# Performance work log

Measured on AMD Instinct MI355X. Metric: run time of the kernel, lower is better.

Reference implementation:

```python
import jax, jax.numpy as jnp
from jax import lax
import numpy as np

B, H, W = 2, 48, 48
C_IN, C_OUT = 96, 192
D_INNER, N_STATE, DT_RANK, K = 192, 16, 6, 4  # VMamba: expand=2, d_state=16, dt_rank=ceil(C/16)
EPS = 1e-5


def setup_inputs() -> dict:
    ks = jax.random.split(jax.random.key(0), 16)
    s = 0.02
    r = lambda k, sh, sc=s: jax.random.normal(k, sh, jnp.float32) * sc
    d, N, R = D_INNER, N_STATE, DT_RANK
    return {
        "x": jax.random.normal(ks[0], (B, C_IN, H, W), jnp.float32),
        "ln_g": jnp.ones((C_IN,), jnp.float32),
        "ln_b": jnp.zeros((C_IN,), jnp.float32),
        "in_proj_w": r(ks[1], (2 * d, C_IN)),
        "dwconv_w": r(ks[2], (d, 1, 3, 3)),
        "dwconv_b": jnp.zeros((d,), jnp.float32),
        "x_proj_w": r(ks[3], (K, R + 2 * N, d)),
        "dt_w": r(ks[4], (K, d, R)),
        "dt_b": r(ks[5], (K, d), 0.1),
        "A_logs": jnp.tile(jnp.log(jnp.arange(1, N + 1, dtype=jnp.float32)), (K, d, 1)),
        "Ds": jnp.ones((K, d), jnp.float32),
        "out_norm_g": jnp.ones((d,), jnp.float32),
        "out_norm_b": jnp.zeros((d,), jnp.float32),
        "out_proj_w": r(ks[6], (C_IN, d)),
        "w1": r(ks[7], (C_OUT, C_IN, 1, 1)),
        "b1": jnp.zeros((C_OUT,), jnp.float32),
        "w31": r(ks[8], (C_OUT, C_IN, 3, 3)),
        "b31": jnp.zeros((C_OUT,), jnp.float32),
        "w32": r(ks[9], (C_OUT, C_IN, 3, 3)),
        "b32": jnp.zeros((C_OUT,), jnp.float32),
        "w33": r(ks[10], (C_OUT, C_OUT, 3, 3)),
        "b33": jnp.zeros((C_OUT,), jnp.float32),
        "bn_g": jnp.ones((3 * C_OUT,), jnp.float32),
        "bn_b": jnp.zeros((3 * C_OUT,), jnp.float32),
        "bn_m": r(ks[11], (3 * C_OUT,), 0.1),
        "bn_v": jax.random.uniform(ks[12], (3 * C_OUT,), jnp.float32) + 0.5,
        "prelu_a": jnp.float32(0.25),
    }


def _layernorm(x, g, b):
    m = jnp.mean(x, -1, keepdims=True)
    v = jnp.var(x, -1, keepdims=True)
    return (x - m) * lax.rsqrt(v + EPS) * g + b


def _conv(x, w, b, stride, pad, groups=1):
    y = lax.conv_general_dilated(x, w, (stride, stride), [(pad, pad), (pad, pad)],
                                 dimension_numbers=("NCHW", "OIHW", "NCHW"),
                                 feature_group_count=groups)
    return y + b[None, :, None, None]


def _ss2d(x, in_proj_w, dwconv_w, dwconv_b, x_proj_w, dt_w, dt_b, A_logs, Ds,
          out_norm_g, out_norm_b, out_proj_w):
    # x: (B, H, W, C)
    Bb, Hh, Ww, C = x.shape
    d, N, R = D_INNER, N_STATE, DT_RANK
    L = Hh * Ww
    xz = jnp.einsum("bhwc,ec->bhwe", x, in_proj_w)  # (B,H,W,2d)
    xin, z = jnp.split(xz, 2, axis=-1)
    xc = jnp.transpose(xin, (0, 3, 1, 2))           # (B,d,H,W)
    xc = jax.nn.silu(_conv(xc, dwconv_w, dwconv_b, 1, 1, groups=d))
    # 4 scan directions: row-major, col-major, and their reverses
    x_flat = xc.reshape(Bb, d, L)
    x_t = jnp.transpose(xc, (0, 1, 3, 2)).reshape(Bb, d, L)
    xs = jnp.stack([x_flat, x_t, x_flat[:, :, ::-1], x_t[:, :, ::-1]], axis=1)  # (B,K,d,L)
    x_dbl = jnp.einsum("bkdl,kcd->bkcl", xs, x_proj_w)
    dts, Bs, Cs = x_dbl[:, :, :R], x_dbl[:, :, R:R + N], x_dbl[:, :, R + N:]
    delta = jax.nn.softplus(jnp.einsum("bkrl,kdr->bkdl", dts, dt_w) + dt_b[None, :, :, None])
    A = -jnp.exp(A_logs)                                   # (K,d,N)
    dA = jnp.exp(jnp.einsum("bkdl,kdn->lbkdn", delta, A))  # (L,B,K,d,N)
    dBu = jnp.einsum("bkdl,bknl,bkdl->lbkdn", delta, Bs, xs)
    Cseq = jnp.transpose(Cs, (3, 0, 1, 2))                 # (L,B,K,N)

    def step(h, inp):
        dA_t, dBu_t, c_t = inp
        h = dA_t * h + dBu_t
        return h, jnp.einsum("bkdn,bkn->bkd", h, c_t)

    h0 = jnp.zeros((Bb, K, d, N), x.dtype)
    _, ys = lax.scan(step, h0, (dA, dBu, Cseq))            # ys: (L,B,K,d)
    ys = jnp.transpose(ys, (1, 2, 3, 0)) + xs * Ds[None, :, :, None]  # (B,K,d,L)

    def t_back(a):  # undo the HW transpose of col-major scans
        return jnp.transpose(a.reshape(Bb, d, Ww, Hh), (0, 1, 3, 2)).reshape(Bb, d, L)

    y = ys[:, 0] + ys[:, 2, :, ::-1] + t_back(ys[:, 1]) + t_back(ys[:, 3, :, ::-1])
    y = _layernorm(jnp.transpose(y, (0, 2, 1)), out_norm_g, out_norm_b).reshape(Bb, Hh, Ww, d)
    y = y * jax.nn.silu(z)
    return jnp.einsum("bhwd,cd->bhwc", y, out_proj_w)


def reference(x, ln_g, ln_b, in_proj_w, dwconv_w, dwconv_b, x_proj_w, dt_w, dt_b,
              A_logs, Ds, out_norm_g, out_norm_b, out_proj_w,
              w1, b1, w31, b31, w32, b32, w33, b33,
              bn_g, bn_b, bn_m, bn_v, prelu_a):
    # VSSBlock: residual + SS2D on LayerNorm'd NHWC features
    x_nhwc = jnp.transpose(x, (0, 2, 3, 1))
    x_nhwc = x_nhwc + _ss2d(_layernorm(x_nhwc, ln_g, ln_b), in_proj_w, dwconv_w,
                            dwconv_b, x_proj_w, dt_w, dt_b, A_logs, Ds,
                            out_norm_g, out_norm_b, out_proj_w)
    xm = jnp.transpose(x_nhwc, (0, 3, 1, 2))  # (B,C,H,W)
    # multi-branch stride-2 downsample
    x1 = _conv(xm, w1, b1, 2, 0)
    x2 = _conv(xm, w31, b31, 2, 1)
    x3 = _conv(_conv(xm, w32, b32, 2, 1), w33, b33, 1, 1)
    out = jnp.concatenate([x1, x2, x3], axis=1)  # (B, 3*C_OUT, H/2, W/2)
    # BatchNorm2d (inference, running stats) + PReLU(single param)
    out = (out - bn_m[None, :, None, None]) * lax.rsqrt(bn_v + EPS)[None, :, None, None] \
          * bn_g[None, :, None, None] + bn_b[None, :, None, None]
    return jnp.where(out > 0, out, prelu_a * out)
```

## Files before the change

### kernel.cpp

```cpp
#include <hip/hip_runtime.h>
#include <math.h>

#define BB_ 2
#define HH 48
#define WW 48
#define LL 2304
#define CIN 96
#define DD 192
#define KK 4
#define NN 16
#define RR 6
#define NCH 96
#define LC 24
#define COUT 192
#define OH 24
#define OW 24
#define OHW 576
#define NPX 1152
#define NTOT 4608
#define EPSF 1e-5f

typedef __attribute__((ext_vector_type(8))) short bf16x8;
typedef __attribute__((ext_vector_type(4))) float f32x4;

__device__ __forceinline__ short f2bf(float f) {
  unsigned u = __float_as_uint(f);
  unsigned r = (u + 0x7fffu + ((u >> 16) & 1u)) >> 16;
  return (short)r;
}

__global__ __launch_bounds__(256) void k_prep(const float* __restrict__ x,
                                              const float* __restrict__ g,
                                              const float* __restrict__ b,
                                              const float* __restrict__ inw,
                                              const float* __restrict__ xpw,
                                              const float* __restrict__ w31,
                                              const float* __restrict__ w32,
                                              const float* __restrict__ w33,
                                              const float* __restrict__ w1,
                                              const float* __restrict__ wout,
                                              float* __restrict__ stats,
                                              short* __restrict__ WgTb,
                                              float* __restrict__ sWg,
                                              float* __restrict__ sWb,
                                              short* __restrict__ At3p,
                                              short* __restrict__ At1b,
                                              short* __restrict__ At2b,
                                              short* __restrict__ woutb,
                                              short* __restrict__ xb) {
  __shared__ float tile[32][33];
  int bx = blockIdx.x;
  int tid = threadIdx.x;
  if (bx < 72) {
    int bb = bx / 36; int l0 = (bx % 36) * 64;
    int p = tid >> 2, q = tid & 3;
    int l = l0 + p;
    const float* xp = x + bb * CIN * LL + l;
    float s = 0.f, ss = 0.f;
    for (int c = q; c < CIN; c += 4) { float v = xp[c * LL]; s += v; ss += v * v; }
    s += __shfl_xor(s, 1, 64); s += __shfl_xor(s, 2, 64);
    ss += __shfl_xor(ss, 1, 64); ss += __shfl_xor(ss, 2, 64);
    if (q == 0) {
      float m = s / CIN; float var = ss / CIN - m * m;
      stats[(bb * LL + l) * 2 + 0] = m;
      stats[(bb * LL + l) * 2 + 1] = rsqrtf(var + EPSF);
    }
  } else if (bx == 72) {
    for (int e = tid; e < 2 * DD; e += 256) {
      float swg = 0.f, swb = 0.f;
      for (int c = 0; c < CIN; c++) {
        float w = inw[e * CIN + c];
        float wg = w * g[c];
        WgTb[e * CIN + c] = f2bf(wg);
        swg += wg; swb += w * b[c];
      }
      sWg[e] = swg; sWb[e] = swb;
    }
  } else if (bx < 217) {
    int idx = (bx - 73) * 256 + tid;
    if (idx < 4 * 48 * 192) {
      int m = idx / 192, d = idx - m * 192;
      int kd = m / 48, r = m - kd * 48;
      At3p[idx] = (r < 38) ? f2bf(xpw[(kd * 38 + r) * 192 + d]) : (short)0;
    }
  } else if (bx < 2161) {
    int i = (bx - 217) * 256 + tid;
    if (i < 497664) {
      float v;
      if (i < 165888) v = w31[i];
      else if (i < 331776) v = w32[i - 165888];
      else {
        int k = i % 864; int m = i / 864 - 384;
        v = (k % 9 == 4) ? w1[m * 96 + k / 9] : 0.f;
      }
      At1b[i] = f2bf(v);
    }
  } else if (bx < 3457) {
    int i = (bx - 2161) * 256 + tid;
    if (i < 331776) At2b[i] = f2bf(w33[i]);
  } else if (bx < 3529) {
    int i = (bx - 3457) * 256 + tid;
    if (i < 18432) woutb[i] = f2bf(wout[i]);
  } else {
    int tt = bx - 3529;
    int bb = tt / 216; int r2 = tt % 216;
    int ct = r2 / 72, lt = r2 % 72;
    int c0 = ct * 32, l0 = lt * 32;
    int r = tid >> 5, cc = tid & 31;
    for (int rr = r; rr < 32; rr += 8)
      tile[rr][cc] = x[(size_t)bb * CIN * LL + (c0 + rr) * LL + l0 + cc];
    __syncthreads();
    for (int rr = r; rr < 32; rr += 8)
      xb[((size_t)bb * LL + l0 + rr) * CIN + c0 + cc] = f2bf(tile[cc][rr]);
  }
}

__global__ __launch_bounds__(256) void k_inprojM(const short* __restrict__ WgTb,
                                                 const short* __restrict__ xb,
                                                 const float* __restrict__ stats,
                                                 const float* __restrict__ sWg,
                                                 const float* __restrict__ sWb,
                                                 float* __restrict__ xin,
                                                 float* __restrict__ z) {
  __shared__ short As[64][40];
  __shared__ short Bs[64][40];
  int n0 = blockIdx.x * 64;
  int m0 = blockIdx.y * 64;
  int tid = threadIdx.x;
  int lane = tid & 63;
  int wv = tid >> 6;
  int row16 = lane & 15;
  int kg = lane >> 4;
  int sm = tid >> 2;
  int sk8 = (tid & 3) * 8;
  f32x4 acc[4];
#pragma unroll
  for (int i = 0; i < 4; i++) acc[i] = (f32x4){0.f, 0.f, 0.f, 0.f};
#pragma unroll
  for (int ks = 0; ks < 96; ks += 32) {
    *(bf16x8*)&As[sm][sk8] = *(const bf16x8*)&WgTb[(size_t)(m0 + sm) * CIN + ks + sk8];
    *(bf16x8*)&Bs[sm][sk8] = *(const bf16x8*)&xb[(size_t)(n0 + sm) * CIN + ks + sk8];
    __syncthreads();
    bf16x8 a = *(const bf16x8*)&As[wv * 16 + row16][kg * 8];
#pragma unroll
    for (int tn = 0; tn < 4; tn++) {
      bf16x8 b = *(const bf16x8*)&Bs[tn * 16 + row16][kg * 8];
      acc[tn] = __builtin_amdgcn_mfma_f32_16x16x32_bf16(a, b, acc[tn], 0, 0, 0);
    }
    __syncthreads();
  }
#pragma unroll
  for (int tn = 0; tn < 4; tn++) {
    int px = n0 + tn * 16 + row16;
    int bb = px / LL, l = px - bb * LL;
    float mm = stats[px * 2], rr = stats[px * 2 + 1];
    int rowb = m0 + wv * 16 + kg * 4;
#pragma unroll
    for (int i = 0; i < 4; i++) {
      int e = rowb + i;
      float v = rr * (acc[tn][i] - mm * sWg[e]) + sWb[e];
      if (e < DD) xin[((size_t)bb * DD + e) * LL + l] = v;
      else z[(size_t)px * DD + (e - DD)] = v;
    }
  }
}

__global__ __launch_bounds__(256) void k_dwconv(const float* __restrict__ xin,
                                                const float* __restrict__ wdw,
                                                const float* __restrict__ bdw,
                                                float* __restrict__ xs,
                                                short* __restrict__ xsb) {
  __shared__ float vt[32 * 50];
  int bid = blockIdx.x;
  int bb = bid / 288; int r = bid % 288; int dg = r / 72; int tile = r % 72;
  int l0 = tile * 32;
  int d0 = dg * 48;
  for (int i = threadIdx.x; i < 32 * 48; i += 256) {
    int lj = i & 31, dl = i >> 5;
    int d = d0 + dl;
    int l = l0 + lj;
    int h = l / WW, w = l % WW;
    const float* xp = xin + (bb * DD + d) * LL;
    const float* wq = wdw + d * 9;
    float acc = bdw[d];
#pragma unroll
    for (int kh = 0; kh < 3; kh++) {
      int ih = h + kh - 1; if (ih < 0 || ih >= HH) continue;
#pragma unroll
      for (int kw = 0; kw < 3; kw++) {
        int iw = w + kw - 1; if (iw < 0 || iw >= WW) continue;
        acc += xp[ih * WW + iw] * wq[kh * 3 + kw];
      }
    }
    float v = acc / (1.f + __expf(-acc));
    vt[lj * 50 + dl] = v;
  }
  __syncthreads();
  for (int j = threadIdx.x; j < 32 * 48; j += 256) {
    int lj = j / 48, dl = j - lj * 48;
    int d = d0 + dl;
    int l = l0 + lj;
    int h = l / WW, w = l % WW;
    int lt = w * HH + h;
    float v = vt[lj * 50 + dl];
    xs[((size_t)(bb * 2 + 0) * LL + l) * DD + d] = v;
    xs[((size_t)(bb * 2 + 1) * LL + lt) * DD + d] = v;
    xsb[((size_t)bb * LL + l) * DD + d] = f2bf(v);
  }
}

__global__ __launch_bounds__(256) void k_xprojF(const short* __restrict__ At3p,
                                                const short* __restrict__ xsb,
                                                const float* __restrict__ dtw,
                                                const float* __restrict__ dtb,
                                                float* __restrict__ Bsb,
                                                float* __restrict__ Csb,
                                                float* __restrict__ delta) {
  __shared__ short As[48][40];
  __shared__ short Bs[64][40];
  __shared__ float ct[38][65];
  int bid = blockIdx.x;
  int kd = bid / 72; int tile = bid % 72;
  int pg0 = tile * 64;
  int bb = pg0 / LL;
  int lbase = pg0 - bb * LL;
  int tid = threadIdx.x;
  int lane = tid & 63;
  int wvn = tid >> 6;
  int row16 = lane & 15;
  int kg = lane >> 4;
  f32x4 acc[3];
#pragma unroll
  for (int j = 0; j < 3; j++) acc[j] = (f32x4){0.f, 0.f, 0.f, 0.f};
  int sm = tid >> 2, sk8 = (tid & 3) * 8;
  for (int ks = 0; ks < 192; ks += 32) {
    if (tid < 192)
      *(bf16x8*)&As[sm][sk8] =
          *(const bf16x8*)&At3p[(size_t)(kd * 48 + sm) * 192 + ks + sk8];
    *(bf16x8*)&Bs[sm][sk8] =
        *(const bf16x8*)&xsb[(size_t)(pg0 + sm) * 192 + ks + sk8];
    __syncthreads();
    bf16x8 b = *(const bf16x8*)&Bs[wvn * 16 + row16][kg * 8];
#pragma unroll
    for (int j = 0; j < 3; j++) {
      bf16x8 a = *(const bf16x8*)&As[j * 16 + row16][kg * 8];
      acc[j] = __builtin_amdgcn_mfma_f32_16x16x32_bf16(a, b, acc[j], 0, 0, 0);
    }
    __syncthreads();
  }
#pragma unroll
  for (int j = 0; j < 3; j++) {
    int rowb = j * 16 + kg * 4;
    int col = wvn * 16 + row16;
#pragma unroll
    for (int i = 0; i < 4; i++)
      if (rowb + i < 38) ct[rowb + i][col] = acc[j][i];
  }
  __syncthreads();
  for (int i = tid; i < 64 * 16; i += 256) {
    int lj = i >> 4, n = i & 15;
    int l = lbase + lj; int h = l / WW, w = l - h * WW; int lt = w * HH + h;
    int pos = (kd == 0) ? l : (kd == 1) ? lt : (kd == 2) ? (LL - 1 - l) : (LL - 1 - lt);
    size_t base = ((size_t)(bb * 4 + kd) * LL + pos) * NN + n;
    Bsb[base] = ct[6 + n][lj];
    Csb[base] = ct[22 + n][lj];
  }
  for (int i = tid; i < 64 * 192; i += 256) {
    int lj = i / 192, d = i - lj * 192;
    int l = lbase + lj; int h = l / WW, w = l - h * WW; int lt = w * HH + h;
    int pos = (kd == 0) ? l : (kd == 1) ? lt : (kd == 2) ? (LL - 1 - l) : (LL - 1 - lt);
    const float* wd = dtw + (kd * DD + d) * RR;
    float a2 = dtb[kd * DD + d];
#pragma unroll
    for (int r = 0; r < RR; r++) a2 += wd[r] * ct[r][lj];
    float sp = a2 > 20.f ? a2 : log1pf(__expf(a2));
    delta[((size_t)(bb * 4 + kd) * LL + pos) * DD + d] = sp;
  }
}

__global__ __launch_bounds__(192) void k_scan1(const float* __restrict__ delta,
                                               const float* __restrict__ xs,
                                               const float* __restrict__ Bsb,
                                               const float* __restrict__ A_logs,
                                               float* __restrict__ Pbuf,
                                               float* __restrict__ Sbuf) {
  __shared__ float Bls[LC * NN];
  int bid = blockIdx.x;
  int c = bid % NCH; int bk = bid / NCH; int k = bk & 3; int bb = bk >> 2;
  int t0 = c * LC;
  int d = threadIdx.x;
  const float* bp = Bsb + ((size_t)bk * LL + t0) * NN;
  for (int i = d; i < LC * NN; i += 192) Bls[i] = bp[i];
  float A[NN];
  {
    const float4* ap = (const float4*)(A_logs + (k * DD + d) * NN);
#pragma unroll
    for (int j = 0; j < 4; j++) {
      float4 a4 = ap[j];
      A[4 * j + 0] = -__expf(a4.x); A[4 * j + 1] = -__expf(a4.y);
      A[4 * j + 2] = -__expf(a4.z); A[4 * j + 3] = -__expf(a4.w);
    }
  }
  bool seq = true;
#pragma unroll
  for (int n = 0; n < NN; n++) seq = seq && (fabsf(A[n] + (float)(n + 1)) < 1e-3f);
  float h[NN];
#pragma unroll
  for (int n = 0; n < NN; n++) h[n] = 0.f;
  float sd = 0.f;
  __syncthreads();
  const float* dp = delta + ((size_t)bk * LL + t0) * DD + d;
  const float* xpb = xs + ((size_t)(bb * 2 + (k & 1)) * LL) * DD + d;
  const float* xp; int xstep;
  if (k < 2) { xp = xpb + (size_t)t0 * DD; xstep = DD; }
  else       { xp = xpb + (size_t)(LL - 1 - t0) * DD; xstep = -DD; }
#pragma unroll 2
  for (int t = 0; t < LC; ++t) {
    float dt = dp[t * DD];
    float xv = xp[t * xstep];
    float u = dt * xv;
    sd += dt;
    float dA[NN];
    if (seq) {
      float q = __expf(-dt);
      float q2 = q * q, q4 = q2 * q2, q8 = q4 * q4;
      dA[0] = q; dA[1] = q2; dA[2] = q2 * q; dA[3] = q4;
      dA[4] = q4 * q; dA[5] = q4 * q2; dA[6] = q4 * dA[2]; dA[7] = q8;
      dA[8] = q8 * q; dA[9] = q8 * q2; dA[10] = q8 * dA[2]; dA[11] = q8 * q4;
      dA[12] = q8 * dA[4]; dA[13] = q8 * dA[5]; dA[14] = q8 * dA[6]; dA[15] = q8 * q8;
    } else {
#pragma unroll
      for (int n = 0; n < NN; n++) dA[n] = __expf(dt * A[n]);
    }
    const float4* b4 = (const float4*)&Bls[t * NN];
#pragma unroll
    for (int j = 0; j < 4; j++) {
      float4 bv = b4[j];
      h[4 * j + 0] = dA[4 * j + 0] * h[4 * j + 0] + u * bv.x;
      h[4 * j + 1] = dA[4 * j + 1] * h[4 * j + 1] + u * bv.y;
      h[4 * j + 2] = dA[4 * j + 2] * h[4 * j + 2] + u * bv.z;
      h[4 * j + 3] = dA[4 * j + 3] * h[4 * j + 3] + u * bv.w;
    }
  }
  int chn = (bk * DD + d) * NN;
  float* pp = Pbuf + (size_t)c * 24576 + chn;
  float* sp = Sbuf + (size_t)c * 24576 + chn;
#pragma unroll
  for (int n = 0; n < NN; n++) { pp[n] = __expf(A[n] * sd); sp[n] = h[n]; }
}

__global__ __launch_bounds__(256) void k_scan2(const float* __restrict__ Pbuf,
                                               const float* __restrict__ Sbuf,
                                               float* __restrict__ Hinit) {
  int idx = blockIdx.x * 256 + threadIdx.x;
  float h = 0.f;
#pragma unroll 4
  for (int c = 0; c < NCH; c++) {
    Hinit[(size_t)c * 24576 + idx] = h;
    h = Pbuf[(size_t)c * 24576 + idx] * h + Sbuf[(size_t)c * 24576 + idx];
  }
}

__global__ __launch_bounds__(192) void k_scan3(const float* __restrict__ delta,
                                               const float* __restrict__ xs,
                                               const float* __restrict__ Bsb,
                                               const float* __restrict__ Csb,
                                               const float* __restrict__ A_logs,
                                               const float* __restrict__ Ds,
                                               const float* __restrict__ Hinit,
                                               float* __restrict__ ys) {
  __shared__ float Bls[LC * NN];
  __shared__ float Cls[LC * NN];
  int bid = blockIdx.x;
  int c = bid % NCH; int bk = bid / NCH; int k = bk & 3; int bb = bk >> 2;
  int t0 = c * LC;
  int d = threadIdx.x;
  const float* bp = Bsb + ((size_t)bk * LL + t0) * NN;
  const float* cp = Csb + ((size_t)bk * LL + t0) * NN;
  for (int i = d; i < LC * NN; i += 192) { Bls[i] = bp[i]; Cls[i] = cp[i]; }
  float A[NN];
  {
    const float4* ap = (const float4*)(A_logs + (k * DD + d) * NN);
#pragma unroll
    for (int j = 0; j < 4; j++) {
      float4 a4 = ap[j];
      A[4 * j + 0] = -__expf(a4.x); A[4 * j + 1] = -__expf(a4.y);
      A[4 * j + 2] = -__expf(a4.z); A[4 * j + 3] = -__expf(a4.w);
    }
  }
  bool seq = true;
#pragma unroll
  for (int n = 0; n < NN; n++) seq = seq && (fabsf(A[n] + (float)(n + 1)) < 1e-3f);
  float Dv = Ds[k * DD + d];
  float h[NN];
  {
    const float4* hp = (const float4*)(Hinit + (size_t)c * 24576 + (bk * DD + d) * NN);
#pragma unroll
    for (int j = 0; j < 4; j++) {
      float4 h4 = hp[j];
      h[4 * j + 0] = h4.x; h[4 * j + 1] = h4.y;
      h[4 * j + 2] = h4.z; h[4 * j + 3] = h4.w;
    }
  }
  __syncthreads();
  const float* dp = delta + ((size_t)bk * LL + t0) * DD + d;
  const float* xpb = xs + ((size_t)(bb * 2 + (k & 1)) * LL) * DD + d;
  const float* xp; int xstep;
  if (k < 2) { xp = xpb + (size_t)t0 * DD; xstep = DD; }
  else       { xp = xpb + (size_t)(LL - 1 - t0) * DD; xstep = -DD; }
  float* yp = ys + ((size_t)bk * LL + t0) * DD + d;
#pragma unroll 2
  for (int t = 0; t < LC; ++t) {
    float dt = dp[t * DD];
    float xv = xp[t * xstep];
    float u = dt * xv;
    float y = 0.f;
    float dA[NN];
    if (seq) {
      float q = __expf(-dt);
      float q2 = q * q, q4 = q2 * q2, q8 = q4 * q4;
      dA[0] = q; dA[1] = q2; dA[2] = q2 * q; dA[3] = q4;
      dA[4] = q4 * q; dA[5] = q4 * q2; dA[6] = q4 * dA[2]; dA[7] = q8;
      dA[8] = q8 * q; dA[9] = q8 * q2; dA[10] = q8 * dA[2]; dA[11] = q8 * q4;
      dA[12] = q8 * dA[4]; dA[13] = q8 * dA[5]; dA[14] = q8 * dA[6]; dA[15] = q8 * q8;
    } else {
#pragma unroll
      for (int n = 0; n < NN; n++) dA[n] = __expf(dt * A[n]);
    }
    const float4* b4 = (const float4*)&Bls[t * NN];
    const float4* c4 = (const float4*)&Cls[t * NN];
#pragma unroll
    for (int j = 0; j < 4; j++) {
      float4 bv = b4[j];
      float4 cc = c4[j];
      h[4 * j + 0] = dA[4 * j + 0] * h[4 * j + 0] + u * bv.x;
      h[4 * j + 1] = dA[4 * j + 1] * h[4 * j + 1] + u * bv.y;
      h[4 * j + 2] = dA[4 * j + 2] * h[4 * j + 2] + u * bv.z;
      h[4 * j + 3] = dA[4 * j + 3] * h[4 * j + 3] + u * bv.w;
      y += h[4 * j + 0] * cc.x + h[4 * j + 1] * cc.y
         + h[4 * j + 2] * cc.z + h[4 * j + 3] * cc.w;
    }
    yp[t * DD] = y + Dv * xv;
  }
}

__global__ __launch_bounds__(256) void k_combineF(const float* __restrict__ ys,
                                                  const float* __restrict__ z,
                                                  const float* __restrict__ ong,
                                                  const float* __restrict__ onb,
                                                  const short* __restrict__ Wbf,
                                                  const float* __restrict__ x,
                                                  float* __restrict__ xm) {
  __shared__ float yt[16 * 194];
  __shared__ unsigned Wlu[96 * 98];
  int bx = blockIdx.x; int bb = bx / 144; int l0 = (bx % 144) * 16;
  int tid = threadIdx.x;
  const unsigned* Wu = (const unsigned*)Wbf;
  for (int i = tid; i < 96 * 96; i += 256) {
    int e = i / 96, d2 = i - e * 96;
    Wlu[e * 98 + d2] = Wu[i];
  }
  for (int i = tid; i < 16 * DD; i += 256) {
    int p = i / DD, d = i - p * DD;
    int l = l0 + p; int h = l / WW, w = l - h * WW;
    int t1 = w * HH + h;
    float v = ys[(((size_t)bb * KK + 0) * LL + l) * DD + d]
            + ys[(((size_t)bb * KK + 1) * LL + t1) * DD + d]
            + ys[(((size_t)bb * KK + 2) * LL + (LL - 1 - l)) * DD + d]
            + ys[(((size_t)bb * KK + 3) * LL + (LL - 1 - t1)) * DD + d];
    yt[p * 194 + d] = v;
  }
  __syncthreads();
  int p = tid >> 4, q = tid & 15;
  int l = l0 + p;
  float s = 0.f, ss = 0.f;
  for (int d = q * 12; d < q * 12 + 12; d++) { float v = yt[p * 194 + d]; s += v; ss += v * v; }
  s += __shfl_xor(s, 1, 64); s += __shfl_xor(s, 2, 64);
  s += __shfl_xor(s, 4, 64); s += __shfl_xor(s, 8, 64);
  ss += __shfl_xor(ss, 1, 64); ss += __shfl_xor(ss, 2, 64);
  ss += __shfl_xor(ss, 4, 64); ss += __shfl_xor(ss, 8, 64);
  float m = s / DD, var = ss / DD - m * m;
  float rr = rsqrtf(var + EPSF);
  const float* zp = z + (size_t)(bb * LL + l) * DD;
  for (int d = q * 12; d < q * 12 + 12; d++) {
    float v = (yt[p * 194 + d] - m) * rr * ong[d] + onb[d];
    float zv = zp[d];
    yt[p * 194 + d] = v * zv / (1.f + __expf(-zv));
  }
  __syncthreads();
  float acc[6];
#pragma unroll
  for (int j = 0; j < 6; j++) acc[j] = 0.f;
  for (int d2 = 0; d2 < 96; d2++) {
    float2 y2 = *(float2*)&yt[p * 194 + 2 * d2];
#pragma unroll
    for (int j = 0; j < 6; j++) {
      unsigned wv = Wlu[(q * 6 + j) * 98 + d2];
      float wlo = __uint_as_float(wv << 16);
      float whi = __uint_as_float(wv & 0xffff0000u);
      acc[j] += y2.x * wlo + y2.y * whi;
    }
  }
#pragma unroll
  for (int j = 0; j < 6; j++) {
    int e = q * 6 + j;
    size_t off = ((size_t)bb * CIN + e) * LL + l;
    xm[off] = x[off] + acc[j];
  }
}

template<int MT, int KTOT, int KCHUNK, int CI, int IH, int STRIDE>
__global__ __launch_bounds__(256) void k_cgemm_mfma(const short* __restrict__ Abf,
                                                    const float* __restrict__ SRC,
                                                    float* __restrict__ Cout) {
  __shared__ short As[64][40];
  __shared__ short Bs[64][40];
  int n0 = blockIdx.x * 64;
  int m0 = blockIdx.y * 64;
  int kz = blockIdx.z;
  int k0 = kz * KCHUNK;
  int tid = threadIdx.x;
  int lane = tid & 63;
  int wv = tid >> 6;
  int row16 = lane & 15;
  int kg = lane >> 4;
  int sm = tid >> 2;
  int sk8 = (tid & 3) * 8;
  int n = n0 + sm;
  int bb = n / OHW; int rem = n - bb * OHW;
  int oh = rem / OW, ow = rem - oh * OW;
  f32x4 acc[4];
#pragma unroll
  for (int i = 0; i < 4; i++) acc[i] = (f32x4){0.f, 0.f, 0.f, 0.f};
  for (int ks = 0; ks < KCHUNK; ks += 32) {
    *(bf16x8*)&As[sm][sk8] =
        *(const bf16x8*)&Abf[(size_t)(m0 + sm) * KTOT + k0 + ks + sk8];
    bf16x8 bvv;
#pragma unroll
    for (int j = 0; j < 8; j++) {
      int k = k0 + ks + sk8 + j;
      int ci = k / 9; int r9 = k - ci * 9;
      int kh = r9 / 3, kw = r9 - kh * 3;
      int ih = STRIDE * oh + kh - 1;
      int iw = STRIDE * ow + kw - 1;
      float v = (ih >= 0 && ih < IH && iw >= 0 && iw < IH)
              ? SRC[((size_t)(bb * CI + ci) * IH + ih) * IH + iw] : 0.f;
      bvv[j] = f2bf(v);
    }
    *(bf16x8*)&Bs[sm][sk8] = bvv;
    __syncthreads();
    bf16x8 a = *(const bf16x8*)&As[wv * 16 + row16][kg * 8];
#pragma unroll
    for (int tn = 0; tn < 4; tn++) {
      bf16x8 b = *(const bf16x8*)&Bs[tn * 16 + row16][kg * 8];
      acc[tn] = __builtin_amdgcn_mfma_f32_16x16x32_bf16(a, b, acc[tn], 0, 0, 0);
    }
    __syncthreads();
  }
#pragma unroll
  for (int tn = 0; tn < 4; tn++) {
    int col = n0 + tn * 16 + row16;
    int rowb = m0 + wv * 16 + kg * 4;
#pragma unroll
    for (int i = 0; i < 4; i++)
      Cout[((size_t)kz * MT + rowb + i) * NPX + col] = acc[tn][i];
  }
}

__global__ __launch_bounds__(256) void k_reduce1(const float* __restrict__ Cp1,
                                                 const float* __restrict__ b1,
                                                 const float* __restrict__ b31,
                                                 const float* __restrict__ b32,
                                                 const float* __restrict__ bn_g,
                                                 const float* __restrict__ bn_b,
                                                 const float* __restrict__ bn_m,
                                                 const float* __restrict__ bn_v,
                                                 const float* __restrict__ prelu_a,
                                                 float* __restrict__ out,
                                                 float* __restrict__ t3) {
  int idx = blockIdx.x * 256 + threadIdx.x;
  if (idx >= 576 * NPX) return;
  int m = idx / NPX, n = idx % NPX;
  float s = 0.f;
#pragma unroll
  for (int c = 0; c < 3; c++) s += Cp1[(size_t)c * 576 * NPX + idx];
  int bb = n / OHW, o = n % OHW;
  if (m < 192) {
    s += b31[m];
    int cc = 192 + m;
    float scale = rsqrtf(bn_v[cc] + EPSF) * bn_g[cc];
    float v = s * scale + (bn_b[cc] - bn_m[cc] * scale);
    float a = prelu_a[0];
    out[((size_t)bb * 576 + cc) * OHW + o] = v > 0.f ? v : a * v;
  } else if (m < 384) {
    s += b32[m - 192];
    t3[((size_t)bb * COUT + (m - 192)) * OHW + o] = s;
  } else {
    s += b1[m - 384];
    int cc = m - 384;
    float scale = rsqrtf(bn_v[cc] + EPSF) * bn_g[cc];
    float v = s * scale + (bn_b[cc] - bn_m[cc] * scale);
    float a = prelu_a[0];
    out[((size_t)bb * 576 + cc) * OHW + o] = v > 0.f ? v : a * v;
  }
}

__global__ __launch_bounds__(256) void k_reduce2(const float* __restrict__ Cp2,
                                                 const float* __restrict__ b33,
                                                 const float* __restrict__ bn_g,
                                                 const float* __restrict__ bn_b,
                                                 const float* __restrict__ bn_m,
                                                 const float* __restrict__ bn_v,
                                                 const float* __restrict__ prelu_a,
                                                 float* __restrict__ out) {
  int idx = blockIdx.x * 256 + threadIdx.x;
  if (idx >= 192 * NPX) return;
  int m = idx / NPX, n = idx % NPX;
  float s = b33[m];
#pragma unroll
  for (int c = 0; c < 6; c++) s += Cp2[(size_t)c * 192 * NPX + idx];
  int bb = n / OHW, o = n % OHW;
  int cc = 384 + m;
  float scale = rsqrtf(bn_v[cc] + EPSF) * bn_g[cc];
  float v = s * scale + (bn_b[cc] - bn_m[cc] * scale);
  float a = prelu_a[0];
  out[((size_t)bb * 576 + cc) * OHW + o] = v > 0.f ? v : a * v;
}

extern "C" void kernel_launch(void* const* d_in, const int* in_sizes, int n_in,
                              void* d_out, int out_size, void* d_ws, size_t ws_size,
                              hipStream_t stream) {
  const float* x        = (const float*)d_in[0];
  const float* ln_g     = (const float*)d_in[1];
  const float* ln_b     = (const float*)d_in[2];
  const float* in_proj_w= (const float*)d_in[3];
  const float* dwconv_w = (const float*)d_in[4];
  const float* dwconv_b = (const float*)d_in[5];
  const float* x_proj_w = (const float*)d_in[6];
  const float* dt_w     = (const float*)d_in[7];
  const float* dt_b     = (const float*)d_in[8];
  const float* A_logs   = (const float*)d_in[9];
  const float* Ds       = (const float*)d_in[10];
  const float* out_norm_g = (const float*)d_in[11];
  const float* out_norm_b = (const float*)d_in[12];
  const float* out_proj_w = (const float*)d_in[13];
  const float* w1  = (const float*)d_in[14];
  const float* b1  = (const float*)d_in[15];
  const float* w31 = (const float*)d_in[16];
  const float* b31 = (const float*)d_in[17];
  const float* w32 = (const float*)d_in[18];
  const float* b32 = (const float*)d_in[19];
  const float* w33 = (const float*)d_in[20];
  const float* b33 = (const float*)d_in[21];
  const float* bn_g = (const float*)d_in[22];
  const float* bn_b = (const float*)d_in[23];
  const float* bn_m = (const float*)d_in[24];
  const float* bn_v = (const float*)d_in[25];
  const float* prelu_a = (const float*)d_in[26];

  float* ws = (float*)d_ws;
  float* stats = ws + 0;
  short* WgTb  = (short*)(ws + 16384);
  float* sWg   = ws + 65536;
  float* sWb   = ws + 66048;
  short* At3p  = (short*)(ws + 98304);
  short* At1b  = (short*)(ws + 147456);
  short* At2b  = (short*)(ws + 397312);
  short* woutb = (short*)(ws + 565248);
  float* xin   = ws + 2097152;
  float* z     = ws + 3145728;
  float* xs    = ws + 4194304;
  short* xsb   = (short*)(ws + 6291456);
  float* delta = ws + 10485760;
  float* Bsb   = ws + 14155776;
  float* Csb   = ws + 14680064;
  float* Pbuf  = ws + 15728640;
  float* Sbuf  = ws + 18874368;
  float* Hinit = ws + 22020096;
  float* ys    = ws + 25165824;
  float* xm    = ws + 29360128;
  float* t3    = ws + 30408704;
  float* Cp1   = ws + 31457280;
  float* Cp2   = ws + 33554432;
  short* xb    = (short*)(ws + 35651584);
  float* out = (float*)d_out;

  k_prep<<<3961, 256, 0, stream>>>(x, ln_g, ln_b, in_proj_w, x_proj_w,
                                   w31, w32, w33, w1, out_proj_w,
                                   stats, WgTb, sWg, sWb, At3p, At1b, At2b,
                                   woutb, xb);
  k_inprojM<<<dim3(72, 6), 256, 0, stream>>>(WgTb, xb, stats, sWg, sWb, xin, z);
  k_dwconv<<<576, 256, 0, stream>>>(xin, dwconv_w, dwconv_b, xs, xsb);
  k_xprojF<<<288, 256, 0, stream>>>(At3p, xsb, dt_w, dt_b, Bsb, Csb, delta);
  k_scan1<<<768, 192, 0, stream>>>(delta, xs, Bsb, A_logs, Pbuf, Sbuf);
  k_scan2<<<96, 256, 0, stream>>>(Pbuf, Sbuf, Hinit);
  k_scan3<<<768, 192, 0, stream>>>(delta, xs, Bsb, Csb, A_logs, Ds, Hinit, ys);
  k_combineF<<<288, 256, 0, stream>>>(ys, z, out_norm_g, out_norm_b, woutb, x, xm);
  k_cgemm_mfma<576, 864, 288, CIN, HH, 2><<<dim3(18, 9, 3), 256, 0, stream>>>(
      At1b, xm, Cp1);
  k_reduce1<<<2592, 256, 0, stream>>>(Cp1, b1, b31, b32, bn_g, bn_b, bn_m, bn_v,
                                      prelu_a, out, t3);
  k_cgemm_mfma<192, 1728, 288, COUT, OH, 1><<<dim3(18, 3, 6), 256, 0, stream>>>(
      At2b, t3, Cp2);
  k_reduce2<<<864, 256, 0, stream>>>(Cp2, b33, bn_g, bn_b, bn_m, bn_v, prelu_a, out);
}
```

Baseline: 190.7 us.

## Fuse conv GEMM epilogues, drop split-K, stage in_proj output through LDS

The two implicit-GEMM convolutions now run over the full K dimension instead of split-K chunks. Bias, BatchNorm and PReLU are applied directly in the GEMM epilogue, which removes the two reduction kernels and the partial-sum buffers. The in_proj GEMM stages its accumulator tile in shared memory so the xin (channel-major) and z (pixel-major) writes are coalesced. The trade-off is fewer blocks for the conv GEMMs (162 and 54 instead of 486 and 324) with a longer serial K loop, which lowers parallelism on a GPU with many CUs.

```diff
diff --git a/kernel.cpp b/kernel.cpp
--- a/kernel.cpp
+++ b/kernel.cpp
@@ -124,6 +124,7 @@
                                                  float* __restrict__ z) {
   __shared__ short As[64][40];
   __shared__ short Bs[64][40];
+  __shared__ float ct[64][65];
   int n0 = blockIdx.x * 64;
   int m0 = blockIdx.y * 64;
   int tid = threadIdx.x;
@@ -151,16 +152,28 @@
   }
 #pragma unroll
   for (int tn = 0; tn < 4; tn++) {
-    int px = n0 + tn * 16 + row16;
-    int bb = px / LL, l = px - bb * LL;
-    float mm = stats[px * 2], rr = stats[px * 2 + 1];
-    int rowb = m0 + wv * 16 + kg * 4;
-#pragma unroll
-    for (int i = 0; i < 4; i++) {
-      int e = rowb + i;
-      float v = rr * (acc[tn][i] - mm * sWg[e]) + sWb[e];
-      if (e < DD) xin[((size_t)bb * DD + e) * LL + l] = v;
-      else z[(size_t)px * DD + (e - DD)] = v;
+    int nl = tn * 16 + row16;
+    int mlb = wv * 16 + kg * 4;
+#pragma unroll
+    for (int i = 0; i < 4; i++) ct[mlb + i][nl] = acc[tn][i];
+  }
+  __syncthreads();
+  if (m0 < DD) {
+    for (int idx = tid; idx < 64 * 64; idx += 256) {
+      int ml = idx >> 6, nl = idx & 63;
+      int e = m0 + ml; int px = n0 + nl;
+      int bb = px / LL, l = px - bb * LL;
+      float mm = stats[px * 2], rr = stats[px * 2 + 1];
+      float v = rr * (ct[ml][nl] - mm * sWg[e]) + sWb[e];
+      xin[((size_t)bb * DD + e) * LL + l] = v;
+    }
+  } else {
+    for (int idx = tid; idx < 64 * 64; idx += 256) {
+      int nl = idx >> 6, ml = idx & 63;
+      int e = m0 + ml; int px = n0 + nl;
+      float mm = stats[px * 2], rr = stats[px * 2 + 1];
+      float v = rr * (ct[ml][nl] - mm * sWg[e]) + sWb[e];
+      z[(size_t)px * DD + (e - DD)] = v;
     }
   }
 }
@@ -509,16 +522,24 @@
   }
 }
 
-template<int MT, int KTOT, int KCHUNK, int CI, int IH, int STRIDE>
+template<int MT, int KTOT, int CI, int IH, int STRIDE, int EPI>
 __global__ __launch_bounds__(256) void k_cgemm_mfma(const short* __restrict__ Abf,
                                                     const float* __restrict__ SRC,
-                                                    float* __restrict__ Cout) {
+                                                    float* __restrict__ out,
+                                                    float* __restrict__ t3,
+                                                    const float* __restrict__ b1,
+                                                    const float* __restrict__ b31,
+                                                    const float* __restrict__ b32,
+                                                    const float* __restrict__ b33,
+                                                    const float* __restrict__ bn_g,
+                                                    const float* __restrict__ bn_b,
+                                                    const float* __restrict__ bn_m,
+                                                    const float* __restrict__ bn_v,
+                                                    const float* __restrict__ prelu_a) {
   __shared__ short As[64][40];
   __shared__ short Bs[64][40];
   int n0 = blockIdx.x * 64;
   int m0 = blockIdx.y * 64;
-  int kz = blockIdx.z;
-  int k0 = kz * KCHUNK;
   int tid = threadIdx.x;
   int lane = tid & 63;
   int wv = tid >> 6;
@@ -526,25 +547,25 @@
   int kg = lane >> 4;
   int sm = tid >> 2;
   int sk8 = (tid & 3) * 8;
-  int n = n0 + sm;
-  int bb = n / OHW; int rem = n - bb * OHW;
-  int oh = rem / OW, ow = rem - oh * OW;
+  int nS = n0 + sm;
+  int bbS = nS / OHW; int remS = nS - bbS * OHW;
+  int ohS = remS / OW, owS = remS - ohS * OW;
   f32x4 acc[4];
 #pragma unroll
   for (int i = 0; i < 4; i++) acc[i] = (f32x4){0.f, 0.f, 0.f, 0.f};
-  for (int ks = 0; ks < KCHUNK; ks += 32) {
+  for (int ks = 0; ks < KTOT; ks += 32) {
     *(bf16x8*)&As[sm][sk8] =
-        *(const bf16x8*)&Abf[(size_t)(m0 + sm) * KTOT + k0 + ks + sk8];
+        *(const bf16x8*)&Abf[(size_t)(m0 + sm) * KTOT + ks + sk8];
     bf16x8 bvv;
 #pragma unroll
     for (int j = 0; j < 8; j++) {
-      int k = k0 + ks + sk8 + j;
+      int k = ks + sk8 + j;
       int ci = k / 9; int r9 = k - ci * 9;
       int kh = r9 / 3, kw = r9 - kh * 3;
-      int ih = STRIDE * oh + kh - 1;
-      int iw = STRIDE * ow + kw - 1;
+      int ih = STRIDE * ohS + kh - 1;
+      int iw = STRIDE * owS + kw - 1;
       float v = (ih >= 0 && ih < IH && iw >= 0 && iw < IH)
-              ? SRC[((size_t)(bb * CI + ci) * IH + ih) * IH + iw] : 0.f;
+              ? SRC[((size_t)(bbS * CI + ci) * IH + ih) * IH + iw] : 0.f;
       bvv[j] = f2bf(v);
     }
     *(bf16x8*)&Bs[sm][sk8] = bvv;
@@ -557,74 +578,41 @@
     }
     __syncthreads();
   }
+  float aslope = prelu_a[0];
 #pragma unroll
   for (int tn = 0; tn < 4; tn++) {
-    int col = n0 + tn * 16 + row16;
+    int n = n0 + tn * 16 + row16;
+    int bb = n / OHW, o = n - bb * OHW;
     int rowb = m0 + wv * 16 + kg * 4;
 #pragma unroll
-    for (int i = 0; i < 4; i++)
-      Cout[((size_t)kz * MT + rowb + i) * NPX + col] = acc[tn][i];
-  }
-}
-
-__global__ __launch_bounds__(256) void k_reduce1(const float* __restrict__ Cp1,
-                                                 const float* __restrict__ b1,
-                                                 const float* __restrict__ b31,
-                                                 const float* __restrict__ b32,
-                                                 const float* __restrict__ bn_g,
-                                                 const float* __restrict__ bn_b,
-                                                 const float* __restrict__ bn_m,
-                                                 const float* __restrict__ bn_v,
-                                                 const float* __restrict__ prelu_a,
-                                                 float* __restrict__ out,
-                                                 float* __restrict__ t3) {
-  int idx = blockIdx.x * 256 + threadIdx.x;
-  if (idx >= 576 * NPX) return;
-  int m = idx / NPX, n = idx % NPX;
-  float s = 0.f;
-#pragma unroll
-  for (int c = 0; c < 3; c++) s += Cp1[(size_t)c * 576 * NPX + idx];
-  int bb = n / OHW, o = n % OHW;
-  if (m < 192) {
-    s += b31[m];
-    int cc = 192 + m;
-    float scale = rsqrtf(bn_v[cc] + EPSF) * bn_g[cc];
-    float v = s * scale + (bn_b[cc] - bn_m[cc] * scale);
-    float a = prelu_a[0];
-    out[((size_t)bb * 576 + cc) * OHW + o] = v > 0.f ? v : a * v;
-  } else if (m < 384) {
-    s += b32[m - 192];
-    t3[((size_t)bb * COUT + (m - 192)) * OHW + o] = s;
-  } else {
-    s += b1[m - 384];
-    int cc = m - 384;
-    float scale = rsqrtf(bn_v[cc] + EPSF) * bn_g[cc];
-    float v = s * scale + (bn_b[cc] - bn_m[cc] * scale);
-    float a = prelu_a[0];
-    out[((size_t)bb * 576 + cc) * OHW + o] = v > 0.f ? v : a * v;
-  }
-}
-
-__global__ __launch_bounds__(256) void k_reduce2(const float* __restrict__ Cp2,
-                                                 const float* __restrict__ b33,
-                                                 const float* __restrict__ bn_g,
-                                                 const float* __restrict__ bn_b,
-                                                 const float* __restrict__ bn_m,
-                                                 const float* __restrict__ bn_v,
-                                                 const float* __restrict__ prelu_a,
-                                                 float* __restrict__ out) {
-  int idx = blockIdx.x * 256 + threadIdx.x;
-  if (idx >= 192 * NPX) return;
-  int m = idx / NPX, n = idx % NPX;
-  float s = b33[m];
-#pragma unroll
-  for (int c = 0; c < 6; c++) s += Cp2[(size_t)c * 192 * NPX + idx];
-  int bb = n / OHW, o = n % OHW;
-  int cc = 384 + m;
-  float scale = rsqrtf(bn_v[cc] + EPSF) * bn_g[cc];
-  float v = s * scale + (bn_b[cc] - bn_m[cc] * scale);
-  float a = prelu_a[0];
-  out[((size_t)bb * 576 + cc) * OHW + o] = v > 0.f ? v : a * v;
+    for (int i = 0; i < 4; i++) {
+      int m = rowb + i;
+      float s = acc[tn][i];
+      if (EPI == 1) {
+        if (m < 192) {
+          int cc = 192 + m;
+          s += b31[m];
+          float scale = rsqrtf(bn_v[cc] + EPSF) * bn_g[cc];
+          float v = s * scale + (bn_b[cc] - bn_m[cc] * scale);
+          out[((size_t)bb * 576 + cc) * OHW + o] = v > 0.f ? v : aslope * v;
+        } else if (m < 384) {
+          t3[((size_t)bb * COUT + (m - 192)) * OHW + o] = s + b32[m - 192];
+        } else {
+          int cc = m - 384;
+          s += b1[cc];
+          float scale = rsqrtf(bn_v[cc] + EPSF) * bn_g[cc];
+          float v = s * scale + (bn_b[cc] - bn_m[cc] * scale);
+          out[((size_t)bb * 576 + cc) * OHW + o] = v > 0.f ? v : aslope * v;
+        }
+      } else {
+        int cc = 384 + m;
+        s += b33[m];
+        float scale = rsqrtf(bn_v[cc] + EPSF) * bn_g[cc];
+        float v = s * scale + (bn_b[cc] - bn_m[cc] * scale);
+        out[((size_t)bb * 576 + cc) * OHW + o] = v > 0.f ? v : aslope * v;
+      }
+    }
+  }
 }
 
 extern "C" void kernel_launch(void* const* d_in, const int* in_sizes, int n_in,
@@ -680,8 +668,6 @@
   float* ys    = ws + 25165824;
   float* xm    = ws + 29360128;
   float* t3    = ws + 30408704;
-  float* Cp1   = ws + 31457280;
-  float* Cp2   = ws + 33554432;
   short* xb    = (short*)(ws + 35651584);
   float* out = (float*)d_out;
 
@@ -696,11 +682,8 @@
   k_scan2<<<96, 256, 0, stream>>>(Pbuf, Sbuf, Hinit);
   k_scan3<<<768, 192, 0, stream>>>(delta, xs, Bsb, Csb, A_logs, Ds, Hinit, ys);
   k_combineF<<<288, 256, 0, stream>>>(ys, z, out_norm_g, out_norm_b, woutb, x, xm);
-  k_cgemm_mfma<576, 864, 288, CIN, HH, 2><<<dim3(18, 9, 3), 256, 0, stream>>>(
-      At1b, xm, Cp1);
-  k_reduce1<<<2592, 256, 0, stream>>>(Cp1, b1, b31, b32, bn_g, bn_b, bn_m, bn_v,
-                                      prelu_a, out, t3);
-  k_cgemm_mfma<192, 1728, 288, COUT, OH, 1><<<dim3(18, 3, 6), 256, 0, stream>>>(
-      At2b, t3, Cp2);
-  k_reduce2<<<864, 256, 0, stream>>>(Cp2, b33, bn_g, bn_b, bn_m, bn_v, prelu_a, out);
-}
+  k_cgemm_mfma<576, 864, CIN, HH, 2, 1><<<dim3(18, 9), 256, 0, stream>>>(
+      At1b, xm, out, t3, b1, b31, b32, b33, bn_g, bn_b, bn_m, bn_v, prelu_a);
+  k_cgemm_mfma<192, 1728, COUT, OH, 1, 2><<<dim3(18, 3), 256, 0, stream>>>(
+      At2b, t3, out, t3, b1, b31, b32, b33, bn_g, bn_b, bn_m, bn_v, prelu_a);
+}
```

Result: slower. 258.7 us (+35.7%).
